# Kernel tuning notes

Measured on AMD Instinct MI355X. Metric: run time of the kernel, lower is better.

## Reference

```python
import jax, jax.numpy as jnp
import numpy as np

B, C, H, W = 4, 64, 64, 64
C8 = C // 8
OC = 64
K9 = 9


def setup_inputs() -> dict:
    key = jax.random.key(0)
    ks = jax.random.split(key, 8)
    x = jax.random.normal(ks[0], (B, C, H, W), dtype=jnp.float32)
    qw = jax.random.normal(ks[1], (C8, C), dtype=jnp.float32) * 0.05   # 1x1 conv weight
    qb = jax.random.normal(ks[2], (C8,), dtype=jnp.float32) * 0.05
    kw = jax.random.normal(ks[3], (C8, C), dtype=jnp.float32) * 0.05
    kb = jax.random.normal(ks[4], (C8,), dtype=jnp.float32) * 0.05
    gamma = jax.random.normal(ks[5], (1,), dtype=jnp.float32) * 0.1
    weight = jax.random.normal(ks[6], (OC, C, K9), dtype=jnp.float32) * 0.05
    bias = jnp.full((OC,), 0.1, dtype=jnp.float32)
    return {"x": x, "qw": qw, "qb": qb, "kw": kw, "kb": kb,
            "gamma": gamma, "weight": weight, "bias": bias}


def reference(x, qw, qb, kw, kb, gamma, weight, bias):
    b, c, h, w = x.shape
    hw = h * w
    # 1x1 convs -> (B, C8, HW)
    xf = x.reshape(b, c, hw)
    q = jnp.einsum('dc,bcn->bdn', qw, xf) + qb[None, :, None]
    k = jnp.einsum('dc,bcn->bdn', kw, xf) + kb[None, :, None]
    # energy[b,t,s] = <key[:,t], query[:,s]>  -> (B, HW, HW)
    energy = jnp.einsum('bdt,bds->bts', k, q)
    # top-9 source positions per target t; the torch boolean-mask gather
    # selects them in ascending index order, so sort the indices.
    _, idx = jax.lax.top_k(energy, K9)          # (B, HW, 9)
    idx = jnp.sort(idx, axis=-1)
    # gather x at selected positions: (B, HW, 9, C)
    x_t = xf.transpose(0, 2, 1)                 # (B, HW, C)
    gathered = jnp.take_along_axis(x_t[:, None, :, :], idx[:, :, :, None], axis=2)
    # out[b,o,j] = sum_{c,k} gathered[b,j,k,c] * weight[o,c,k] + bias[o]
    out = jnp.einsum('bjkc,ock->boj', gathered, weight) + bias[None, :, None]
    out = jax.nn.relu(out).reshape(b, c, h, w)
    return gamma[0] * out + x
```

## Files before the change

### kernel.cpp

```cpp
#include <hip/hip_runtime.h>
#include <math.h>

#define HW 4096
#define NB 4
#define LCAP 64

typedef unsigned short ushort_t;
typedef unsigned int uint_t;
typedef __attribute__((ext_vector_type(8))) _Float16 f16x8;
typedef __attribute__((ext_vector_type(4))) float f32x4;

__device__ __forceinline__ ushort_t f2h(float f) {
  _Float16 h = (_Float16)f;
  return *(ushort_t*)&h;
}

__device__ __forceinline__ float dot8(float4 klo, float4 khi, const float* qp) {
  float4 q0 = *(const float4*)qp;
  float4 q1 = *(const float4*)(qp + 4);
  float e = klo.x * q0.x;
  e = fmaf(klo.y, q0.y, e);
  e = fmaf(klo.z, q0.z, e);
  e = fmaf(klo.w, q0.w, e);
  e = fmaf(khi.x, q1.x, e);
  e = fmaf(khi.y, q1.y, e);
  e = fmaf(khi.z, q1.z, e);
  e = fmaf(khi.w, q1.w, e);
  return e;
}
__device__ __forceinline__ float dot8v(float4 klo, float4 khi, float4 q0, float4 q1) {
  float e = klo.x * q0.x;
  e = fmaf(klo.y, q0.y, e);
  e = fmaf(klo.z, q0.z, e);
  e = fmaf(klo.w, q0.w, e);
  e = fmaf(khi.x, q1.x, e);
  e = fmaf(khi.y, q1.y, e);
  e = fmaf(khi.z, q1.z, e);
  e = fmaf(khi.w, q1.w, e);
  return e;
}

__global__ __launch_bounds__(256) void qk_kernel(
    const float* __restrict__ x, const float* __restrict__ qw,
    const float* __restrict__ qb, const float* __restrict__ kw,
    const float* __restrict__ kb, const float* __restrict__ w,
    float* __restrict__ q_t, float* __restrict__ k_t,
    ushort_t* __restrict__ xT, ushort_t* __restrict__ wt_h) {
  __shared__ float red[4][64][17];
  __shared__ float sqwT[512], skwT[512];
  int b = blockIdx.y;
  int sl = threadIdx.x & 63;
  int cg = threadIdx.x >> 6;
  int s = blockIdx.x * 64 + sl;

  {
    int bid = blockIdx.y * 64 + blockIdx.x;
    int gid = bid * 256 + threadIdx.x;
    if (gid < 64 * 64 * 9) {
      int o = gid / 576, rem = gid % 576, c = rem / 9, k = rem % 9;
      wt_h[(k * 64 + o) * 64 + c] = f2h(w[gid]);
    }
  }

  for (int i = threadIdx.x; i < 512; i += 256) {
    int c = i >> 3, d = i & 7;
    sqwT[i] = qw[d * 64 + c];
    skwT[i] = kw[d * 64 + c];
  }
  __syncthreads();

  float qa[8], ka[8];
  ushort_t h16[16];
#pragma unroll
  for (int d = 0; d < 8; ++d) { qa[d] = 0.f; ka[d] = 0.f; }
  const float* xp = x + ((size_t)b * 64 + cg * 16) * HW + s;
#pragma unroll
  for (int c = 0; c < 16; ++c) {
    float xv = xp[(size_t)c * HW];
    h16[c] = f2h(xv);
    int cc = cg * 16 + c;
    const float4 qw0 = *(const float4*)&sqwT[cc * 8];
    const float4 qw1 = *(const float4*)&sqwT[cc * 8 + 4];
    const float4 kw0 = *(const float4*)&skwT[cc * 8];
    const float4 kw1 = *(const float4*)&skwT[cc * 8 + 4];
    qa[0] = fmaf(qw0.x, xv, qa[0]); qa[1] = fmaf(qw0.y, xv, qa[1]);
    qa[2] = fmaf(qw0.z, xv, qa[2]); qa[3] = fmaf(qw0.w, xv, qa[3]);
    qa[4] = fmaf(qw1.x, xv, qa[4]); qa[5] = fmaf(qw1.y, xv, qa[5]);
    qa[6] = fmaf(qw1.z, xv, qa[6]); qa[7] = fmaf(qw1.w, xv, qa[7]);
    ka[0] = fmaf(kw0.x, xv, ka[0]); ka[1] = fmaf(kw0.y, xv, ka[1]);
    ka[2] = fmaf(kw0.z, xv, ka[2]); ka[3] = fmaf(kw0.w, xv, ka[3]);
    ka[4] = fmaf(kw1.x, xv, ka[4]); ka[5] = fmaf(kw1.y, xv, ka[5]);
    ka[6] = fmaf(kw1.z, xv, ka[6]); ka[7] = fmaf(kw1.w, xv, ka[7]);
  }
  {
    ushort_t* xo = xT + (((size_t)b * HW + s) * 64 + cg * 16);
    *(uint4*)&xo[0] = *(const uint4*)&h16[0];
    *(uint4*)&xo[8] = *(const uint4*)&h16[8];
  }
#pragma unroll
  for (int d = 0; d < 8; ++d) {
    red[cg][sl][d] = qa[d];
    red[cg][sl][8 + d] = ka[d];
  }
  __syncthreads();

#pragma unroll
  for (int r = 0; r < 4; ++r) {
    int f = r * 256 + threadIdx.x;
    int slf = f >> 4, dd = f & 15;
    float sum = red[0][slf][dd] + red[1][slf][dd] + red[2][slf][dd] + red[3][slf][dd];
    int ss_ = blockIdx.x * 64 + slf;
    if (dd < 8)
      q_t[((size_t)b * HW + ss_) * 8 + dd] = sum + qb[dd];
    else
      k_t[((size_t)b * HW + ss_) * 8 + (dd - 8)] = sum + kb[dd - 8];
  }
}

__global__ __launch_bounds__(256) void mid_kernel(
    const float* __restrict__ q_t, const float* __restrict__ k_t,
    float* __restrict__ maxima) {
  __shared__ float qs[512];
  int blk = blockIdx.x;
  int tid = threadIdx.x;
  int b = blk >> 8;
  int rem = blk & 255;
  int ch = rem >> 2;
  int tg = rem & 3;
  int lane = tid & 63;
  int w = tid >> 6;
  int t0 = tg * 1024 + w * 256 + 4 * lane;

  const float* kp = k_t + ((size_t)b * HW + t0) * 8;
  float4 ka0 = *(const float4*)(kp);      float4 ka1 = *(const float4*)(kp + 4);
  float4 kb0 = *(const float4*)(kp + 8);  float4 kb1 = *(const float4*)(kp + 12);
  float4 kc0 = *(const float4*)(kp + 16); float4 kc1 = *(const float4*)(kp + 20);
  float4 kd0 = *(const float4*)(kp + 24); float4 kd1 = *(const float4*)(kp + 28);

  if (tid < 128)
    *(float4*)&qs[tid * 4] =
        *(const float4*)&q_t[((size_t)b * HW + ch * 64) * 8 + tid * 4];
  __syncthreads();

  float m0 = -INFINITY, m1 = -INFINITY, m2 = -INFINITY, m3 = -INFINITY;
#pragma unroll 4
  for (int i = 0; i < 64; ++i) {
    float4 q0 = *(const float4*)&qs[i * 8];
    float4 q1 = *(const float4*)&qs[i * 8 + 4];
    m0 = fmaxf(m0, dot8v(ka0, ka1, q0, q1));
    m1 = fmaxf(m1, dot8v(kb0, kb1, q0, q1));
    m2 = fmaxf(m2, dot8v(kc0, kc1, q0, q1));
    m3 = fmaxf(m3, dot8v(kd0, kd1, q0, q1));
  }
  *(float4*)&maxima[((size_t)b * 64 + ch) * HW + t0] =
      make_float4(m0, m1, m2, m3);
}

__global__ __launch_bounds__(1024, 4) void topk_gather_kernel(
    const float* __restrict__ q_t, const float* __restrict__ k_t,
    const float* __restrict__ maxima, const ushort_t* __restrict__ xT,
    const ushort_t* __restrict__ wt_h, const float* __restrict__ bias,
    const float* __restrict__ gamma, const float* __restrict__ x,
    float* __restrict__ out) {
  __shared__ float ldsM[64 * 17];
  __shared__ int sArr[16][LCAP];
  __shared__ float eArr[16][LCAP];
  __shared__ int sIdx[16][9];
  __shared__ float T[64 * 17];
  __shared__ __align__(16) ushort_t Gf[16 * 648];
  int b = blockIdx.y;
  int tid = threadIdx.x;
  int lane = tid & 63;
  int w = tid >> 6;
  int t0 = blockIdx.x * 16;
  int t = t0 + w;

  {
    int ch = tid >> 4, dt = tid & 15;
    ldsM[ch * 17 + dt] = maxima[((size_t)b * 64 + ch) * HW + t0 + dt];
  }
  __syncthreads();

  float val = ldsM[lane * 17 + w];
  int rnk = 0;
#pragma unroll
  for (int ch = 0; ch < 64; ++ch)
    rnk += (ldsM[ch * 17 + w] > val) ? 1 : 0;
  float tv = (rnk < 9) ? val : INFINITY;
#pragma unroll
  for (int off = 1; off < 64; off <<= 1)
    tv = fminf(tv, __shfl_xor(tv, off, 64));
  float tauv = tv;

  const float* kp = k_t + ((size_t)b * HW + t) * 8;
  float4 klo = *(const float4*)kp;
  float4 khi = *(const float4*)(kp + 4);

  unsigned long long mask = __ballot(val >= tauv);
  int cnt = 0;
#pragma unroll 1
  while (mask) {
    int nbp = (int)__popcll(mask);
    int nb = nbp < 9 ? nbp : 9;
    int id0 = (int)__builtin_ctzll(mask);
    int ids[9];
    unsigned long long m2 = mask;
#pragma unroll
    for (int i = 0; i < 9; ++i) {
      ids[i] = m2 ? (int)__builtin_ctzll(m2) : id0;
      m2 &= (m2 - 1);
    }
    mask = m2;
    float ev[9];
#pragma unroll
    for (int i = 0; i < 9; ++i)
      ev[i] = dot8(klo, khi, q_t + ((size_t)b * HW + ids[i] * 64 + lane) * 8);
#pragma unroll
    for (int i = 0; i < 9; ++i) {
      if (i < nb) {
        bool keep = ev[i] >= tauv;
        unsigned long long km = __ballot(keep);
        if (keep) {
          int pos = cnt + (int)__popcll(km & ((1ull << lane) - 1ull));
          if (pos < LCAP) {
            sArr[w][pos] = ids[i] * 64 + lane;
            eArr[w][pos] = ev[i];
          }
        }
        cnt += (int)__popcll(km);
      }
    }
  }
  if (cnt > LCAP) cnt = LCAP;

  {
    float em = -INFINITY; int sm = 0x7fffffff;
    if (lane < cnt) { em = eArr[w][lane]; sm = sArr[w][lane]; }
    int rank = 0;
    for (int i = 0; i < cnt; ++i) {
      float ei = eArr[w][i];
      int si = sArr[w][i];
      rank += ((ei > em) || (ei == em && si < sm)) ? 1 : 0;
    }
    bool sel = (lane < cnt) && (rank < 9);
    unsigned long long smask = __ballot(sel);
    int pos = (int)__popcll(smask & ((1ull << lane) - 1ull));
    if (sel) sIdx[w][pos] = sm;
  }

  {
    const ushort_t* xTb = xT + (size_t)b * HW * 64;
#pragma unroll
    for (int i = 0; i < 3; ++i) {
      int idx = i * 64 + lane;
      if (idx < 144) {
        int k = idx >> 4, sub = idx & 15;
        int p = sIdx[w][k];
        *(uint2*)&Gf[w * 648 + k * 72 + sub * 4] =
            *(const uint2*)&xTb[(size_t)p * 64 + sub * 4];
      }
    }
  }
  __syncthreads();

  if (w < 4) {
    int lr = lane & 15, lg = lane >> 4;
    f32x4 acc = {0.f, 0.f, 0.f, 0.f};
    const ushort_t* wbase = wt_h + ((size_t)(w * 16 + lr)) * 64 + lg * 8;
#pragma unroll
    for (int k = 0; k < 9; ++k) {
      f16x8 a0 = *(const f16x8*)&Gf[lr * 648 + k * 72 + lg * 8];
      f16x8 a1 = *(const f16x8*)&Gf[lr * 648 + k * 72 + 32 + lg * 8];
      f16x8 b0 = *(const f16x8*)&wbase[(size_t)k * 4096];
      f16x8 b1 = *(const f16x8*)&wbase[(size_t)k * 4096 + 32];
      acc = __builtin_amdgcn_mfma_f32_16x16x32_f16(a0, b0, acc, 0, 0, 0);
      acc = __builtin_amdgcn_mfma_f32_16x16x32_f16(a1, b1, acc, 0, 0, 0);
    }
    float g = gamma[0];
    float bo = bias[w * 16 + lr];
#pragma unroll
    for (int r = 0; r < 4; ++r)
      T[(w * 16 + lr) * 17 + lg * 4 + r] = g * fmaxf(acc[r] + bo, 0.f);
  }
  __syncthreads();

  {
    int o = tid >> 4, jl = tid & 15;
    size_t gi = ((size_t)b * 64 + o) * HW + t0 + jl;
    out[gi] = T[o * 17 + jl] + x[gi];
  }
}

extern "C" void kernel_launch(void* const* d_in, const int* in_sizes, int n_in,
                              void* d_out, int out_size, void* d_ws, size_t ws_size,
                              hipStream_t stream) {
  const float* x = (const float*)d_in[0];
  const float* qw = (const float*)d_in[1];
  const float* qb = (const float*)d_in[2];
  const float* kw = (const float*)d_in[3];
  const float* kb = (const float*)d_in[4];
  const float* gamma = (const float*)d_in[5];
  const float* weight = (const float*)d_in[6];
  const float* bias = (const float*)d_in[7];
  float* out = (float*)d_out;

  char* ws = (char*)d_ws;
  float* q_t = (float*)(ws);
  float* k_t = (float*)(ws + 524288);
  float* maxima = (float*)(ws + 1048576);
  ushort_t* xT = (ushort_t*)(ws + 5242880);
  ushort_t* wt_h = (ushort_t*)(ws + 7340032);

  hipLaunchKernelGGL(qk_kernel, dim3(64, 4), dim3(256), 0, stream,
                     x, qw, qb, kw, kb, weight, q_t, k_t, xT, wt_h);
  hipLaunchKernelGGL(mid_kernel, dim3(1024), dim3(256), 0, stream,
                     q_t, k_t, maxima);
  hipLaunchKernelGGL(topk_gather_kernel, dim3(256, 4), dim3(1024), 0, stream,
                     q_t, k_t, maxima, xT, wt_h, bias, gamma, x, out);
}
```

Before: 126.8 us.

## Share candidate query chunks across waves via LDS in topk gather

Each of the 16 waves in a block publishes its candidate-chunk mask. The block takes the union and stages the query vectors of up to 16 chunks at a time into shared memory, which reuses the old Gf buffer space. Waves then read the chunks they need from LDS instead of each loading them separately from global memory. This trades redundant global loads for extra block-wide barriers and serialised per-chunk loops, and wave divergence in candidate count may now stall the whole block.

```diff
diff --git a/kernel.cpp b/kernel.cpp
--- a/kernel.cpp
+++ b/kernel.cpp
@@ -15,19 +15,6 @@
   return *(ushort_t*)&h;
 }
 
-__device__ __forceinline__ float dot8(float4 klo, float4 khi, const float* qp) {
-  float4 q0 = *(const float4*)qp;
-  float4 q1 = *(const float4*)(qp + 4);
-  float e = klo.x * q0.x;
-  e = fmaf(klo.y, q0.y, e);
-  e = fmaf(klo.z, q0.z, e);
-  e = fmaf(klo.w, q0.w, e);
-  e = fmaf(khi.x, q1.x, e);
-  e = fmaf(khi.y, q1.y, e);
-  e = fmaf(khi.z, q1.z, e);
-  e = fmaf(khi.w, q1.w, e);
-  return e;
-}
 __device__ __forceinline__ float dot8v(float4 klo, float4 khi, float4 q0, float4 q1) {
   float e = klo.x * q0.x;
   e = fmaf(klo.y, q0.y, e);
@@ -167,7 +154,12 @@
   __shared__ float eArr[16][LCAP];
   __shared__ int sIdx[16][9];
   __shared__ float T[64 * 17];
-  __shared__ __align__(16) ushort_t Gf[16 * 648];
+  __shared__ unsigned long long wmaskS[16];
+  __shared__ __align__(16) char scratch[32768];
+  float4* qsl = (float4*)scratch;
+  float4* qsh = (float4*)(scratch + 16384);
+  ushort_t* Gf = (ushort_t*)scratch;
+
   int b = blockIdx.y;
   int tid = threadIdx.x;
   int lane = tid & 63;
@@ -192,44 +184,60 @@
     tv = fminf(tv, __shfl_xor(tv, off, 64));
   float tauv = tv;
 
+  unsigned long long mymask = __ballot(val >= tauv);
+  if (lane == 0) wmaskS[w] = mymask;
+
   const float* kp = k_t + ((size_t)b * HW + t) * 8;
   float4 klo = *(const float4*)kp;
   float4 khi = *(const float4*)(kp + 4);
-
-  unsigned long long mask = __ballot(val >= tauv);
+  __syncthreads();
+
+  unsigned long long um = 0;
+#pragma unroll
+  for (int i = 0; i < 16; ++i) um |= wmaskS[i];
+
   int cnt = 0;
+  unsigned long long rem = um;
 #pragma unroll 1
-  while (mask) {
-    int nbp = (int)__popcll(mask);
-    int nb = nbp < 9 ? nbp : 9;
-    int id0 = (int)__builtin_ctzll(mask);
-    int ids[9];
-    unsigned long long m2 = mask;
-#pragma unroll
-    for (int i = 0; i < 9; ++i) {
-      ids[i] = m2 ? (int)__builtin_ctzll(m2) : id0;
-      m2 &= (m2 - 1);
-    }
-    mask = m2;
-    float ev[9];
-#pragma unroll
-    for (int i = 0; i < 9; ++i)
-      ev[i] = dot8(klo, khi, q_t + ((size_t)b * HW + ids[i] * 64 + lane) * 8);
-#pragma unroll
-    for (int i = 0; i < 9; ++i) {
-      if (i < nb) {
-        bool keep = ev[i] >= tauv;
-        unsigned long long km = __ballot(keep);
-        if (keep) {
-          int pos = cnt + (int)__popcll(km & ((1ull << lane) - 1ull));
-          if (pos < LCAP) {
-            sArr[w][pos] = ids[i] * 64 + lane;
-            eArr[w][pos] = ev[i];
-          }
+  while (rem) {
+    unsigned long long tmp = rem;
+#pragma unroll
+    for (int i = 0; i < 16; ++i) { if (tmp) tmp &= tmp - 1; }
+    unsigned long long grp = rem ^ tmp;
+    rem = tmp;
+    int ng = (int)__popcll(grp);
+
+    if (w < ng) {
+      unsigned long long g2 = grp;
+      for (int i = 0; i < w; ++i) g2 &= g2 - 1;
+      int cid = (int)__builtin_ctzll(g2);
+      const float* qp = q_t + ((size_t)b * HW + cid * 64 + lane) * 8;
+      qsl[w * 64 + lane] = *(const float4*)qp;
+      qsh[w * 64 + lane] = *(const float4*)(qp + 4);
+    }
+    __syncthreads();
+
+    unsigned long long my = mymask & grp;
+#pragma unroll 1
+    while (my) {
+      int c = (int)__builtin_ctzll(my);
+      my &= my - 1;
+      int slot = (int)__popcll(grp & ((1ull << c) - 1ull));
+      float4 q0 = qsl[slot * 64 + lane];
+      float4 q1 = qsh[slot * 64 + lane];
+      float e = dot8v(klo, khi, q0, q1);
+      bool keep = e >= tauv;
+      unsigned long long km = __ballot(keep);
+      if (keep) {
+        int pos = cnt + (int)__popcll(km & ((1ull << lane) - 1ull));
+        if (pos < LCAP) {
+          sArr[w][pos] = c * 64 + lane;
+          eArr[w][pos] = e;
         }
-        cnt += (int)__popcll(km);
       }
-    }
+      cnt += (int)__popcll(km);
+    }
+    __syncthreads();
   }
   if (cnt > LCAP) cnt = LCAP;
 
```

Result: no change. 127.3 us (+0.4%).

## Fuse chunk-maxima computation into top-k kernel and scan all sources in two passes

Applied to the files above, without the earlier changes.

Removes the separate mid_kernel that wrote per-chunk energy maxima to global memory. Each wave of the top-k kernel now computes its own 64 chunk maxima directly, with one lane per residue class, derives the 9th-largest threshold, then does a second full pass over all 4096 sources to collect candidates above it. This drops one launch and the round trip of the maxima buffer. In exchange every target recomputes all energies twice instead of only rescanning the selected chunks, so per-target arithmetic and q_t reads roughly double versus the previous sparse rescan.

```diff
diff --git a/kernel.cpp b/kernel.cpp
--- a/kernel.cpp
+++ b/kernel.cpp
@@ -15,19 +15,6 @@
   return *(ushort_t*)&h;
 }
 
-__device__ __forceinline__ float dot8(float4 klo, float4 khi, const float* qp) {
-  float4 q0 = *(const float4*)qp;
-  float4 q1 = *(const float4*)(qp + 4);
-  float e = klo.x * q0.x;
-  e = fmaf(klo.y, q0.y, e);
-  e = fmaf(klo.z, q0.z, e);
-  e = fmaf(klo.w, q0.w, e);
-  e = fmaf(khi.x, q1.x, e);
-  e = fmaf(khi.y, q1.y, e);
-  e = fmaf(khi.z, q1.z, e);
-  e = fmaf(khi.w, q1.w, e);
-  return e;
-}
 __device__ __forceinline__ float dot8v(float4 klo, float4 khi, float4 q0, float4 q1) {
   float e = klo.x * q0.x;
   e = fmaf(klo.y, q0.y, e);
@@ -117,52 +104,11 @@
   }
 }
 
-__global__ __launch_bounds__(256) void mid_kernel(
-    const float* __restrict__ q_t, const float* __restrict__ k_t,
-    float* __restrict__ maxima) {
-  __shared__ float qs[512];
-  int blk = blockIdx.x;
-  int tid = threadIdx.x;
-  int b = blk >> 8;
-  int rem = blk & 255;
-  int ch = rem >> 2;
-  int tg = rem & 3;
-  int lane = tid & 63;
-  int w = tid >> 6;
-  int t0 = tg * 1024 + w * 256 + 4 * lane;
-
-  const float* kp = k_t + ((size_t)b * HW + t0) * 8;
-  float4 ka0 = *(const float4*)(kp);      float4 ka1 = *(const float4*)(kp + 4);
-  float4 kb0 = *(const float4*)(kp + 8);  float4 kb1 = *(const float4*)(kp + 12);
-  float4 kc0 = *(const float4*)(kp + 16); float4 kc1 = *(const float4*)(kp + 20);
-  float4 kd0 = *(const float4*)(kp + 24); float4 kd1 = *(const float4*)(kp + 28);
-
-  if (tid < 128)
-    *(float4*)&qs[tid * 4] =
-        *(const float4*)&q_t[((size_t)b * HW + ch * 64) * 8 + tid * 4];
-  __syncthreads();
-
-  float m0 = -INFINITY, m1 = -INFINITY, m2 = -INFINITY, m3 = -INFINITY;
-#pragma unroll 4
-  for (int i = 0; i < 64; ++i) {
-    float4 q0 = *(const float4*)&qs[i * 8];
-    float4 q1 = *(const float4*)&qs[i * 8 + 4];
-    m0 = fmaxf(m0, dot8v(ka0, ka1, q0, q1));
-    m1 = fmaxf(m1, dot8v(kb0, kb1, q0, q1));
-    m2 = fmaxf(m2, dot8v(kc0, kc1, q0, q1));
-    m3 = fmaxf(m3, dot8v(kd0, kd1, q0, q1));
-  }
-  *(float4*)&maxima[((size_t)b * 64 + ch) * HW + t0] =
-      make_float4(m0, m1, m2, m3);
-}
-
 __global__ __launch_bounds__(1024, 4) void topk_gather_kernel(
     const float* __restrict__ q_t, const float* __restrict__ k_t,
-    const float* __restrict__ maxima, const ushort_t* __restrict__ xT,
-    const ushort_t* __restrict__ wt_h, const float* __restrict__ bias,
-    const float* __restrict__ gamma, const float* __restrict__ x,
-    float* __restrict__ out) {
-  __shared__ float ldsM[64 * 17];
+    const ushort_t* __restrict__ xT, const ushort_t* __restrict__ wt_h,
+    const float* __restrict__ bias, const float* __restrict__ gamma,
+    const float* __restrict__ x, float* __restrict__ out) {
   __shared__ int sArr[16][LCAP];
   __shared__ float eArr[16][LCAP];
   __shared__ int sIdx[16][9];
@@ -175,61 +121,48 @@
   int t0 = blockIdx.x * 16;
   int t = t0 + w;
 
-  {
-    int ch = tid >> 4, dt = tid & 15;
-    ldsM[ch * 17 + dt] = maxima[((size_t)b * 64 + ch) * HW + t0 + dt];
-  }
-  __syncthreads();
-
-  float val = ldsM[lane * 17 + w];
+  const float* kp = k_t + ((size_t)b * HW + t) * 8;
+  float4 klo = *(const float4*)kp;
+  float4 khi = *(const float4*)(kp + 4);
+  const float* qbase = q_t + ((size_t)b * HW + lane) * 8;
+
+  float m = -INFINITY;
+#pragma unroll 4
+  for (int i = 0; i < 64; ++i) {
+    const float* qp = qbase + (size_t)i * 512;
+    float4 q0 = *(const float4*)qp;
+    float4 q1 = *(const float4*)(qp + 4);
+    m = fmaxf(m, dot8v(klo, khi, q0, q1));
+  }
+
+  eArr[w][lane] = m;
   int rnk = 0;
 #pragma unroll
-  for (int ch = 0; ch < 64; ++ch)
-    rnk += (ldsM[ch * 17 + w] > val) ? 1 : 0;
-  float tv = (rnk < 9) ? val : INFINITY;
+  for (int j = 0; j < 64; ++j)
+    rnk += (eArr[w][j] > m) ? 1 : 0;
+  float tv = (rnk < 9) ? m : INFINITY;
 #pragma unroll
   for (int off = 1; off < 64; off <<= 1)
     tv = fminf(tv, __shfl_xor(tv, off, 64));
   float tauv = tv;
 
-  const float* kp = k_t + ((size_t)b * HW + t) * 8;
-  float4 klo = *(const float4*)kp;
-  float4 khi = *(const float4*)(kp + 4);
-
-  unsigned long long mask = __ballot(val >= tauv);
   int cnt = 0;
-#pragma unroll 1
-  while (mask) {
-    int nbp = (int)__popcll(mask);
-    int nb = nbp < 9 ? nbp : 9;
-    int id0 = (int)__builtin_ctzll(mask);
-    int ids[9];
-    unsigned long long m2 = mask;
-#pragma unroll
-    for (int i = 0; i < 9; ++i) {
-      ids[i] = m2 ? (int)__builtin_ctzll(m2) : id0;
-      m2 &= (m2 - 1);
-    }
-    mask = m2;
-    float ev[9];
-#pragma unroll
-    for (int i = 0; i < 9; ++i)
-      ev[i] = dot8(klo, khi, q_t + ((size_t)b * HW + ids[i] * 64 + lane) * 8);
-#pragma unroll
-    for (int i = 0; i < 9; ++i) {
-      if (i < nb) {
-        bool keep = ev[i] >= tauv;
-        unsigned long long km = __ballot(keep);
-        if (keep) {
-          int pos = cnt + (int)__popcll(km & ((1ull << lane) - 1ull));
-          if (pos < LCAP) {
-            sArr[w][pos] = ids[i] * 64 + lane;
-            eArr[w][pos] = ev[i];
-          }
-        }
-        cnt += (int)__popcll(km);
+#pragma unroll 2
+  for (int i = 0; i < 64; ++i) {
+    const float* qp = qbase + (size_t)i * 512;
+    float4 q0 = *(const float4*)qp;
+    float4 q1 = *(const float4*)(qp + 4);
+    float e = dot8v(klo, khi, q0, q1);
+    bool keep = e >= tauv;
+    unsigned long long km = __ballot(keep);
+    if (keep) {
+      int pos = cnt + (int)__popcll(km & ((1ull << lane) - 1ull));
+      if (pos < LCAP) {
+        sArr[w][pos] = i * 64 + lane;
+        eArr[w][pos] = e;
       }
     }
+    cnt += (int)__popcll(km);
   }
   if (cnt > LCAP) cnt = LCAP;
 
@@ -307,14 +240,11 @@
   char* ws = (char*)d_ws;
   float* q_t = (float*)(ws);
   float* k_t = (float*)(ws + 524288);
-  float* maxima = (float*)(ws + 1048576);
-  ushort_t* xT = (ushort_t*)(ws + 5242880);
-  ushort_t* wt_h = (ushort_t*)(ws + 7340032);
+  ushort_t* xT = (ushort_t*)(ws + 1048576);
+  ushort_t* wt_h = (ushort_t*)(ws + 3145728);
 
   hipLaunchKernelGGL(qk_kernel, dim3(64, 4), dim3(256), 0, stream,
                      x, qw, qb, kw, kb, weight, q_t, k_t, xT, wt_h);
-  hipLaunchKernelGGL(mid_kernel, dim3(1024), dim3(256), 0, stream,
-                     q_t, k_t, maxima);
   hipLaunchKernelGGL(topk_gather_kernel, dim3(256, 4), dim3(1024), 0, stream,
-                     q_t, k_t, maxima, xT, wt_h, bias, gamma, x, out);
-}
+                     q_t, k_t, xT, wt_h, bias, gamma, x, out);
+}
```

After: 203.0 us. 1.6x slower.

## Split top-k selection and gathered conv into separate kernels

Applied to the files above, without the earlier changes.

The fused top-k/gather/MFMA kernel is split in two. The top-k kernel now writes the 9 selected indices per target to a workspace buffer. A new 256-thread kernel reads them back, gathers the x rows, runs the MFMA conv and writes the output. This frees the top-k kernel of the gather and conv LDS buffers and of the phases where only 4 of 16 waves work, which may improve occupancy. In exchange it adds a kernel launch and a global round trip for the indices.

```diff
diff --git a/kernel.cpp b/kernel.cpp
--- a/kernel.cpp
+++ b/kernel.cpp
@@ -156,18 +156,12 @@
       make_float4(m0, m1, m2, m3);
 }
 
-__global__ __launch_bounds__(1024, 4) void topk_gather_kernel(
+__global__ __launch_bounds__(1024, 4) void topk_kernel(
     const float* __restrict__ q_t, const float* __restrict__ k_t,
-    const float* __restrict__ maxima, const ushort_t* __restrict__ xT,
-    const ushort_t* __restrict__ wt_h, const float* __restrict__ bias,
-    const float* __restrict__ gamma, const float* __restrict__ x,
-    float* __restrict__ out) {
+    const float* __restrict__ maxima, int* __restrict__ gsidx) {
   __shared__ float ldsM[64 * 17];
   __shared__ int sArr[16][LCAP];
   __shared__ float eArr[16][LCAP];
-  __shared__ int sIdx[16][9];
-  __shared__ float T[64 * 17];
-  __shared__ __align__(16) ushort_t Gf[16 * 648];
   int b = blockIdx.y;
   int tid = threadIdx.x;
   int lane = tid & 63;
@@ -245,25 +239,44 @@
     bool sel = (lane < cnt) && (rank < 9);
     unsigned long long smask = __ballot(sel);
     int pos = (int)__popcll(smask & ((1ull << lane) - 1ull));
-    if (sel) sIdx[w][pos] = sm;
-  }
+    if (sel) gsidx[((size_t)b * HW + t) * 9 + pos] = sm;
+  }
+}
+
+__global__ __launch_bounds__(256) void gconv_kernel(
+    const int* __restrict__ gsidx, const ushort_t* __restrict__ xT,
+    const ushort_t* __restrict__ wt_h, const float* __restrict__ bias,
+    const float* __restrict__ gamma, const float* __restrict__ x,
+    float* __restrict__ out) {
+  __shared__ int sIdx[16][9];
+  __shared__ float T[64 * 17];
+  __shared__ __align__(16) ushort_t Gf[16 * 648];
+  int b = blockIdx.y;
+  int tid = threadIdx.x;
+  int lane = tid & 63;
+  int w = tid >> 6;
+  int t0 = blockIdx.x * 16;
+
+  if (tid < 144)
+    sIdx[tid / 9][tid % 9] = gsidx[((size_t)b * HW + t0 + tid / 9) * 9 + tid % 9];
+  __syncthreads();
 
   {
     const ushort_t* xTb = xT + (size_t)b * HW * 64;
 #pragma unroll
-    for (int i = 0; i < 3; ++i) {
-      int idx = i * 64 + lane;
-      if (idx < 144) {
-        int k = idx >> 4, sub = idx & 15;
-        int p = sIdx[w][k];
-        *(uint2*)&Gf[w * 648 + k * 72 + sub * 4] =
-            *(const uint2*)&xTb[(size_t)p * 64 + sub * 4];
-      }
-    }
-  }
-  __syncthreads();
-
-  if (w < 4) {
+    for (int i = 0; i < 9; ++i) {
+      int pr = i * 256 + tid;
+      int pair = pr >> 4;
+      int sub = pr & 15;
+      int t = pair / 9, k = pair - t * 9;
+      int p = sIdx[t][k];
+      *(uint2*)&Gf[t * 648 + k * 72 + sub * 4] =
+          *(const uint2*)&xTb[(size_t)p * 64 + sub * 4];
+    }
+  }
+  __syncthreads();
+
+  {
     int lr = lane & 15, lg = lane >> 4;
     f32x4 acc = {0.f, 0.f, 0.f, 0.f};
     const ushort_t* wbase = wt_h + ((size_t)(w * 16 + lr)) * 64 + lg * 8;
@@ -284,8 +297,8 @@
   }
   __syncthreads();
 
-  {
-    int o = tid >> 4, jl = tid & 15;
+  for (int f = tid; f < 1024; f += 256) {
+    int o = f >> 4, jl = f & 15;
     size_t gi = ((size_t)b * 64 + o) * HW + t0 + jl;
     out[gi] = T[o * 17 + jl] + x[gi];
   }
@@ -310,11 +323,14 @@
   float* maxima = (float*)(ws + 1048576);
   ushort_t* xT = (ushort_t*)(ws + 5242880);
   ushort_t* wt_h = (ushort_t*)(ws + 7340032);
+  int* gsidx = (int*)(ws + 7413760);
 
   hipLaunchKernelGGL(qk_kernel, dim3(64, 4), dim3(256), 0, stream,
                      x, qw, qb, kw, kb, weight, q_t, k_t, xT, wt_h);
   hipLaunchKernelGGL(mid_kernel, dim3(1024), dim3(256), 0, stream,
                      q_t, k_t, maxima);
-  hipLaunchKernelGGL(topk_gather_kernel, dim3(256, 4), dim3(1024), 0, stream,
-                     q_t, k_t, maxima, xT, wt_h, bias, gamma, x, out);
-}
+  hipLaunchKernelGGL(topk_kernel, dim3(256, 4), dim3(1024), 0, stream,
+                     q_t, k_t, maxima, gsidx);
+  hipLaunchKernelGGL(gconv_kernel, dim3(256, 4), dim3(256), 0, stream,
+                     gsidx, xT, wt_h, bias, gamma, x, out);
+}
```

Measured after the change: 125.7 us. No clear change (-0.9%).
